# Optimization experiments

Measured on AMD Instinct MI355X. Metric: run time of the kernel, lower is better.

The kernel has to match this reference:

```python
import jax, jax.numpy as jnp
import numpy as np

B, C, H, T = 256, 2048, 1024, 64  # batch, code_num, hidden_dim, max_len


def setup_inputs() -> dict:
    key = jax.random.key(0)
    ks = jax.random.split(key, 7)
    s_ih = 1.0 / np.sqrt(C)
    s_hh = 1.0 / np.sqrt(H)
    return {
        "noise": jax.random.normal(ks[0], (B, H), dtype=jnp.float32),
        "W_ih": jax.random.uniform(ks[1], (3 * H, C), jnp.float32, -s_ih, s_ih),
        "b_ih": jax.random.uniform(ks[2], (3 * H,), jnp.float32, -s_ih, s_ih),
        "W_hh": jax.random.uniform(ks[3], (3 * H, H), jnp.float32, -s_hh, s_hh),
        "b_hh": jax.random.uniform(ks[4], (3 * H,), jnp.float32, -s_hh, s_hh),
        "W_out": jax.random.uniform(ks[5], (C, H), jnp.float32, -s_hh, s_hh),
        "b_out": jax.random.uniform(ks[6], (C,), jnp.float32, -s_hh, s_hh),
        "max_len": T,
    }


def reference(noise, W_ih, b_ih, W_hh, b_hh, W_out, b_out, max_len):
    # initial codes = sigmoid(Linear(noise))
    codes0 = jax.nn.sigmoid(noise @ W_out.T + b_out)  # [B, C]
    h0 = jnp.zeros((noise.shape[0], W_hh.shape[1]), dtype=noise.dtype)  # [B, H]

    def step(carry, _):
        codes, h = carry
        gi = codes @ W_ih.T + b_ih           # [B, 3H]
        gh = h @ W_hh.T + b_hh               # [B, 3H]
        i_r, i_z, i_n = jnp.split(gi, 3, axis=-1)
        h_r, h_z, h_n = jnp.split(gh, 3, axis=-1)
        r = jax.nn.sigmoid(i_r + h_r)
        z = jax.nn.sigmoid(i_z + h_z)
        n = jnp.tanh(i_n + r * h_n)
        h_new = (1.0 - z) * n + z * h        # PyTorch GRUCell update
        logits = h_new @ W_out.T + b_out
        codes_new = jax.nn.sigmoid(logits)
        # sample at step t is codes BEFORE the cell; hidden is h AFTER
        return (codes_new, h_new), (codes, h_new)

    _, (samples, hiddens) = jax.lax.scan(step, (codes0, h0), None, length=max_len)
    samples = jnp.swapaxes(samples, 0, 1)  # [B, T, C]
    hiddens = jnp.swapaxes(hiddens, 0, 1)  # [B, T, H]
    return samples, hiddens
```

## Files before the change

### kernel.cpp

```cpp
#include <hip/hip_runtime.h>
#include <hip/hip_bf16.h>

#define BB 256
#define CC 2048
#define HD 1024
#define TT 64
#define H3 3072

typedef __attribute__((ext_vector_type(8))) short bf16x8;
typedef __attribute__((ext_vector_type(4))) float f32x4;

__device__ __forceinline__ float sigmoidf_(float x){ return 1.0f/(1.0f+__expf(-x)); }
__device__ __forceinline__ float tanhf_(float x){ float e=__expf(2.0f*x); return 1.0f - 2.0f/(e+1.0f); }

__device__ __forceinline__ bf16x8 ldfrag(const __hip_bfloat16* p){
  return *reinterpret_cast<const bf16x8*>(p);
}
__device__ __forceinline__ unsigned short bfbits(float x){
  __hip_bfloat16 b = __float2bfloat16(x);
  return *reinterpret_cast<unsigned short*>(&b);
}

__global__ void cvt_f32_bf16(const float* __restrict__ in, __hip_bfloat16* __restrict__ out, int n){
  int i = (blockIdx.x*blockDim.x + threadIdx.x)*4;
  int stride = gridDim.x*blockDim.x*4;
  for (; i < n; i += stride){
    float4 v = *reinterpret_cast<const float4*>(in + i);
    ushort4 s;
    s.x = bfbits(v.x); s.y = bfbits(v.y); s.z = bfbits(v.z); s.w = bfbits(v.w);
    *reinterpret_cast<ushort4*>(out + i) = s;
  }
}

__global__ __launch_bounds__(1024, 4) void cell_kernel(
    const __hip_bfloat16* __restrict__ codes,
    const __hip_bfloat16* __restrict__ hprev,
    const __hip_bfloat16* __restrict__ Wih,
    const __hip_bfloat16* __restrict__ Whh,
    const float* __restrict__ bih,
    const float* __restrict__ bhh,
    float* __restrict__ hiddens,
    __hip_bfloat16* __restrict__ hnext,
    int t, int first)
{
  __shared__ float red[8*64*25];

  const int tid  = threadIdx.x;
  const int lane = tid & 63;
  const int wid  = tid >> 6;
  const int ws   = wid & 3;
  const int kc   = wid >> 2;
  const int bm   = blockIdx.x & 3;
  const int bj   = blockIdx.x >> 2;
  const int m0   = bm*64 + ws*16;
  const int j0   = bj*16;
  const int rl   = lane & 15;
  const int kg   = lane >> 4;

  const __hip_bfloat16* arow = codes + (size_t)(m0+rl)*CC + kc*512 + kg*8;
  const __hip_bfloat16* wr   = Wih   + (size_t)(j0+rl)*CC + kc*512 + kg*8;
  const __hip_bfloat16* wz   = wr + (size_t)HD*CC;
  const __hip_bfloat16* wn   = wz + (size_t)HD*CC;

  f32x4 zz4 = {0.f,0.f,0.f,0.f};
  f32x4 a0=zz4, a1=zz4, a2=zz4, a3=zz4, a4=zz4, a5=zz4;

#pragma unroll 4
  for (int k = 0; k < 512; k += 32){
    bf16x8 a  = ldfrag(arow + k);
    bf16x8 fr = ldfrag(wr + k);
    bf16x8 fz = ldfrag(wz + k);
    bf16x8 fn = ldfrag(wn + k);
    a0 = __builtin_amdgcn_mfma_f32_16x16x32_bf16(a, fr, a0, 0, 0, 0);
    a1 = __builtin_amdgcn_mfma_f32_16x16x32_bf16(a, fz, a1, 0, 0, 0);
    a2 = __builtin_amdgcn_mfma_f32_16x16x32_bf16(a, fn, a2, 0, 0, 0);
  }

  if (!first){
    const __hip_bfloat16* hrow = hprev + (size_t)(m0+rl)*HD + kc*256 + kg*8;
    const __hip_bfloat16* vr   = Whh   + (size_t)(j0+rl)*HD + kc*256 + kg*8;
    const __hip_bfloat16* vz   = vr + (size_t)HD*HD;
    const __hip_bfloat16* vn   = vz + (size_t)HD*HD;
#pragma unroll 4
    for (int k = 0; k < 256; k += 32){
      bf16x8 a  = ldfrag(hrow + k);
      bf16x8 fr = ldfrag(vr + k);
      bf16x8 fz = ldfrag(vz + k);
      bf16x8 fn = ldfrag(vn + k);
      a3 = __builtin_amdgcn_mfma_f32_16x16x32_bf16(a, fr, a3, 0, 0, 0);
      a4 = __builtin_amdgcn_mfma_f32_16x16x32_bf16(a, fz, a4, 0, 0, 0);
      a5 = __builtin_amdgcn_mfma_f32_16x16x32_bf16(a, fn, a5, 0, 0, 0);
    }
  }

  if (kc >= 2){
    float* p = &red[((kc-2)*4 + ws)*64*25 + lane*25];
#pragma unroll
    for (int q = 0; q < 4; q++){
      p[q] = a0[q]; p[4+q] = a1[q]; p[8+q] = a2[q];
      p[12+q] = a3[q]; p[16+q] = a4[q]; p[20+q] = a5[q];
    }
  }
  __syncthreads();
  if (kc < 2){
    const float* p = &red[(kc*4 + ws)*64*25 + lane*25];
#pragma unroll
    for (int q = 0; q < 4; q++){
      a0[q] += p[q]; a1[q] += p[4+q]; a2[q] += p[8+q];
      a3[q] += p[12+q]; a4[q] += p[16+q]; a5[q] += p[20+q];
    }
  }
  __syncthreads();
  if (kc == 1){
    float* p = &red[ws*64*25 + lane*25];
#pragma unroll
    for (int q = 0; q < 4; q++){
      p[q] = a0[q]; p[4+q] = a1[q]; p[8+q] = a2[q];
      p[12+q] = a3[q]; p[16+q] = a4[q]; p[20+q] = a5[q];
    }
  }
  __syncthreads();
  if (kc == 0){
    const float* p = &red[ws*64*25 + lane*25];
#pragma unroll
    for (int q = 0; q < 4; q++){
      a0[q] += p[q]; a1[q] += p[4+q]; a2[q] += p[8+q];
      a3[q] += p[12+q]; a4[q] += p[16+q]; a5[q] += p[20+q];
    }

    const int j = j0 + rl;
    const float bir = bih[j], biz = bih[j+HD], bin = bih[j+2*HD];
    const float bhr = bhh[j], bhz = bhh[j+HD], bhn = bhh[j+2*HD];
    const int rbase = m0 + kg*4;
#pragma unroll
    for (int q = 0; q < 4; q++){
      const int brow = rbase + q;
      float ir = a0[q] + bir, iz = a1[q] + biz, inn = a2[q] + bin;
      float hr = a3[q] + bhr, hz = a4[q] + bhz, hn = a5[q] + bhn;
      float r = sigmoidf_(ir + hr);
      float z = sigmoidf_(iz + hz);
      float n = tanhf_(inn + r*hn);
      float hp = first ? 0.0f : __bfloat162float(hprev[(size_t)brow*HD + j]);
      float hv = (1.0f - z)*n + z*hp;
      hiddens[(size_t)brow*TT*HD + (size_t)t*HD + j] = hv;
      hnext[(size_t)brow*HD + j] = __float2bfloat16(hv);
    }
  }
}

__global__ __launch_bounds__(1024, 4) void logits_kernel(
    const __hip_bfloat16* __restrict__ act,
    const __hip_bfloat16* __restrict__ Wout,
    const float* __restrict__ bout,
    float* __restrict__ samples,
    __hip_bfloat16* __restrict__ codes_out,
    int t)
{
  __shared__ float red[12*64*9];

  const int tid  = threadIdx.x;
  const int lane = tid & 63;
  const int wid  = tid >> 6;
  const int ws   = wid & 3;
  const int kc   = wid >> 2;
  const int bm   = blockIdx.x & 3;
  const int bc   = blockIdx.x >> 2;
  const int m0   = bm*64 + ws*16;
  const int c0   = bc*32;
  const int rl   = lane & 15;
  const int kg   = lane >> 4;

  const __hip_bfloat16* arow = act  + (size_t)(m0+rl)*HD + kc*256 + kg*8;
  const __hip_bfloat16* w0   = Wout + (size_t)(c0+rl)*HD + kc*256 + kg*8;
  const __hip_bfloat16* w1   = w0 + (size_t)16*HD;

  f32x4 zz4 = {0.f,0.f,0.f,0.f};
  f32x4 acc0 = zz4, acc1 = zz4;

#pragma unroll 4
  for (int k = 0; k < 256; k += 32){
    bf16x8 a  = ldfrag(arow + k);
    bf16x8 f0 = ldfrag(w0 + k);
    bf16x8 f1 = ldfrag(w1 + k);
    acc0 = __builtin_amdgcn_mfma_f32_16x16x32_bf16(a, f0, acc0, 0, 0, 0);
    acc1 = __builtin_amdgcn_mfma_f32_16x16x32_bf16(a, f1, acc1, 0, 0, 0);
  }

  if (kc >= 1){
    float* p = &red[((kc-1)*4 + ws)*64*9 + lane*9];
#pragma unroll
    for (int q = 0; q < 4; q++){ p[q] = acc0[q]; p[4+q] = acc1[q]; }
  }
  __syncthreads();
  if (kc == 0){
#pragma unroll
    for (int s = 0; s < 3; s++){
      const float* p = &red[(s*4 + ws)*64*9 + lane*9];
#pragma unroll
      for (int q = 0; q < 4; q++){ acc0[q] += p[q]; acc1[q] += p[4+q]; }
    }

    const int ca = c0 + rl, cb = ca + 16;
    const float b0 = bout[ca], b1 = bout[cb];
    const int rbase = m0 + kg*4;
#pragma unroll
    for (int q = 0; q < 4; q++){
      const int brow = rbase + q;
      float s0 = sigmoidf_(acc0[q] + b0);
      float s1 = sigmoidf_(acc1[q] + b1);
      samples[(size_t)brow*TT*CC + (size_t)t*CC + ca] = s0;
      samples[(size_t)brow*TT*CC + (size_t)t*CC + cb] = s1;
      codes_out[(size_t)brow*CC + ca] = __float2bfloat16(s0);
      codes_out[(size_t)brow*CC + cb] = __float2bfloat16(s1);
    }
  }
}

extern "C" void kernel_launch(void* const* d_in, const int* in_sizes, int n_in,
                              void* d_out, int out_size, void* d_ws, size_t ws_size,
                              hipStream_t stream) {
  const float* noise = (const float*)d_in[0];
  const float* W_ih  = (const float*)d_in[1];
  const float* b_ih  = (const float*)d_in[2];
  const float* W_hh  = (const float*)d_in[3];
  const float* b_hh  = (const float*)d_in[4];
  const float* W_out = (const float*)d_in[5];
  const float* b_out = (const float*)d_in[6];

  float* samples = (float*)d_out;
  float* hiddens = samples + (size_t)BB*TT*CC;

  char* w = (char*)d_ws;
  __hip_bfloat16* wih16 = (__hip_bfloat16*)w;  w += (size_t)H3*CC*2;
  __hip_bfloat16* whh16 = (__hip_bfloat16*)w;  w += (size_t)H3*HD*2;
  __hip_bfloat16* wout16= (__hip_bfloat16*)w;  w += (size_t)CC*HD*2;
  __hip_bfloat16* noise16=(__hip_bfloat16*)w;  w += (size_t)BB*HD*2;
  __hip_bfloat16* codes16=(__hip_bfloat16*)w;  w += (size_t)BB*CC*2;
  __hip_bfloat16* h16a  = (__hip_bfloat16*)w;  w += (size_t)BB*HD*2;
  __hip_bfloat16* h16b  = (__hip_bfloat16*)w;  w += (size_t)BB*HD*2;

  cvt_f32_bf16<<<2048, 256, 0, stream>>>(W_ih,  wih16,  H3*CC);
  cvt_f32_bf16<<<2048, 256, 0, stream>>>(W_hh,  whh16,  H3*HD);
  cvt_f32_bf16<<<1024, 256, 0, stream>>>(W_out, wout16, CC*HD);
  cvt_f32_bf16<<<256,  256, 0, stream>>>(noise, noise16, BB*HD);

  logits_kernel<<<256, 1024, 0, stream>>>(noise16, wout16, b_out, samples, codes16, 0);

  for (int t = 0; t < TT; t++){
    __hip_bfloat16* hprev = (t & 1) ? h16a : h16b;
    __hip_bfloat16* hnext = (t & 1) ? h16b : h16a;
    cell_kernel<<<256, 1024, 0, stream>>>(codes16, hprev, wih16, whh16,
                                          b_ih, b_hh, hiddens, hnext,
                                          t, (t == 0) ? 1 : 0);
    if (t < TT-1){
      logits_kernel<<<256, 1024, 0, stream>>>(hnext, wout16, b_out,
                                              samples, codes16, t+1);
    }
  }
}
```

Baseline: 3.796 ms.

## Fuse per-step GRU and logits kernels into one persistent kernel with grid barriers

Replaces about 128 separate launches of the cell and logits kernels with a single persistent kernel of 256 blocks. The kernel loops over time steps and separates phases with a software grid barrier built on atomics. Block indexing changes so each block owns a fixed batch tile and column slice, which keeps its bias loads in registers across steps. This is meant to remove kernel launch overhead and inter-kernel gaps. It relies on all 256 blocks being co-resident (one per CU on MI355X), otherwise the barrier deadlocks, and the barrier itself adds spin latency.

```diff
diff --git a/kernel.cpp b/kernel.cpp
--- a/kernel.cpp
+++ b/kernel.cpp
@@ -6,13 +6,13 @@
 #define HD 1024
 #define TT 64
 #define H3 3072
+#define NBLK 256
 
 typedef __attribute__((ext_vector_type(8))) short bf16x8;
 typedef __attribute__((ext_vector_type(4))) float f32x4;
 
 __device__ __forceinline__ float sigmoidf_(float x){ return 1.0f/(1.0f+__expf(-x)); }
 __device__ __forceinline__ float tanhf_(float x){ float e=__expf(2.0f*x); return 1.0f - 2.0f/(e+1.0f); }
-
 __device__ __forceinline__ bf16x8 ldfrag(const __hip_bfloat16* p){
   return *reinterpret_cast<const bf16x8*>(p);
 }
@@ -32,16 +32,40 @@
   }
 }
 
-__global__ __launch_bounds__(1024, 4) void cell_kernel(
-    const __hip_bfloat16* __restrict__ codes,
-    const __hip_bfloat16* __restrict__ hprev,
-    const __hip_bfloat16* __restrict__ Wih,
-    const __hip_bfloat16* __restrict__ Whh,
+__device__ __forceinline__ void gridbar(unsigned* cnt, unsigned* gen){
+  __syncthreads();
+  if (threadIdx.x == 0){
+    __threadfence();
+    unsigned g = __hip_atomic_load(gen, __ATOMIC_RELAXED, __HIP_MEMORY_SCOPE_AGENT);
+    unsigned a = __hip_atomic_fetch_add(cnt, 1u, __ATOMIC_ACQ_REL, __HIP_MEMORY_SCOPE_AGENT);
+    if (a == NBLK-1u){
+      __hip_atomic_store(cnt, 0u, __ATOMIC_RELAXED, __HIP_MEMORY_SCOPE_AGENT);
+      __hip_atomic_store(gen, g+1u, __ATOMIC_RELEASE, __HIP_MEMORY_SCOPE_AGENT);
+    } else {
+      while (__hip_atomic_load(gen, __ATOMIC_RELAXED, __HIP_MEMORY_SCOPE_AGENT) == g){
+        __builtin_amdgcn_s_sleep(2);
+      }
+    }
+    __threadfence();
+  }
+  __syncthreads();
+}
+
+#define MFMA(a,b,c) __builtin_amdgcn_mfma_f32_16x16x32_bf16((a),(b),(c),0,0,0)
+
+__global__ __launch_bounds__(1024, 4) void gru_persistent(
+    const __hip_bfloat16* __restrict__ wih,
+    const __hip_bfloat16* __restrict__ whh,
+    const __hip_bfloat16* __restrict__ wout,
+    const __hip_bfloat16* __restrict__ noise16,
     const float* __restrict__ bih,
     const float* __restrict__ bhh,
+    const float* __restrict__ bout,
+    float* __restrict__ samples,
     float* __restrict__ hiddens,
-    __hip_bfloat16* __restrict__ hnext,
-    int t, int first)
+    __hip_bfloat16* codes16,
+    __hip_bfloat16* h16a, __hip_bfloat16* h16b,
+    unsigned* bar)
 {
   __shared__ float red[8*64*25];
 
@@ -50,168 +74,157 @@
   const int wid  = tid >> 6;
   const int ws   = wid & 3;
   const int kc   = wid >> 2;
-  const int bm   = blockIdx.x & 3;
-  const int bj   = blockIdx.x >> 2;
+  const int bm   = blockIdx.x >> 6;
+  const int bsub = blockIdx.x & 63;
   const int m0   = bm*64 + ws*16;
-  const int j0   = bj*16;
   const int rl   = lane & 15;
   const int kg   = lane >> 4;
-
-  const __hip_bfloat16* arow = codes + (size_t)(m0+rl)*CC + kc*512 + kg*8;
-  const __hip_bfloat16* wr   = Wih   + (size_t)(j0+rl)*CC + kc*512 + kg*8;
-  const __hip_bfloat16* wz   = wr + (size_t)HD*CC;
-  const __hip_bfloat16* wn   = wz + (size_t)HD*CC;
-
-  f32x4 zz4 = {0.f,0.f,0.f,0.f};
-  f32x4 a0=zz4, a1=zz4, a2=zz4, a3=zz4, a4=zz4, a5=zz4;
-
-#pragma unroll 4
-  for (int k = 0; k < 512; k += 32){
-    bf16x8 a  = ldfrag(arow + k);
-    bf16x8 fr = ldfrag(wr + k);
-    bf16x8 fz = ldfrag(wz + k);
-    bf16x8 fn = ldfrag(wn + k);
-    a0 = __builtin_amdgcn_mfma_f32_16x16x32_bf16(a, fr, a0, 0, 0, 0);
-    a1 = __builtin_amdgcn_mfma_f32_16x16x32_bf16(a, fz, a1, 0, 0, 0);
-    a2 = __builtin_amdgcn_mfma_f32_16x16x32_bf16(a, fn, a2, 0, 0, 0);
-  }
-
-  if (!first){
-    const __hip_bfloat16* hrow = hprev + (size_t)(m0+rl)*HD + kc*256 + kg*8;
-    const __hip_bfloat16* vr   = Whh   + (size_t)(j0+rl)*HD + kc*256 + kg*8;
-    const __hip_bfloat16* vz   = vr + (size_t)HD*HD;
-    const __hip_bfloat16* vn   = vz + (size_t)HD*HD;
+  unsigned* cnt = bar;
+  unsigned* gen = bar + 32;
+
+  const int jA  = bsub*16 + rl;
+  const int caB = bsub*32 + rl;
+  const int cbB = caB + 16;
+  const float bir = bih[jA], biz = bih[jA+HD], bin = bih[jA+2*HD];
+  const float bhr = bhh[jA], bhz = bhh[jA+HD], bhn = bhh[jA+2*HD];
+  const float b0 = bout[caB], b1 = bout[cbB];
+  const int rbase = m0 + kg*4;
+
+  auto phaseB = [&](const __hip_bfloat16* act, int t){
+    const __hip_bfloat16* arow = act  + (size_t)(m0+rl)*HD + kc*256 + kg*8;
+    const __hip_bfloat16* w0   = wout + (size_t)(bsub*32+rl)*HD + kc*256 + kg*8;
+    const __hip_bfloat16* w1   = w0 + (size_t)16*HD;
+    f32x4 acc0 = {0.f,0.f,0.f,0.f}, acc1 = {0.f,0.f,0.f,0.f};
 #pragma unroll 4
     for (int k = 0; k < 256; k += 32){
-      bf16x8 a  = ldfrag(hrow + k);
-      bf16x8 fr = ldfrag(vr + k);
-      bf16x8 fz = ldfrag(vz + k);
-      bf16x8 fn = ldfrag(vn + k);
-      a3 = __builtin_amdgcn_mfma_f32_16x16x32_bf16(a, fr, a3, 0, 0, 0);
-      a4 = __builtin_amdgcn_mfma_f32_16x16x32_bf16(a, fz, a4, 0, 0, 0);
-      a5 = __builtin_amdgcn_mfma_f32_16x16x32_bf16(a, fn, a5, 0, 0, 0);
-    }
-  }
-
-  if (kc >= 2){
-    float* p = &red[((kc-2)*4 + ws)*64*25 + lane*25];
-#pragma unroll
-    for (int q = 0; q < 4; q++){
-      p[q] = a0[q]; p[4+q] = a1[q]; p[8+q] = a2[q];
-      p[12+q] = a3[q]; p[16+q] = a4[q]; p[20+q] = a5[q];
-    }
-  }
-  __syncthreads();
-  if (kc < 2){
-    const float* p = &red[(kc*4 + ws)*64*25 + lane*25];
-#pragma unroll
-    for (int q = 0; q < 4; q++){
-      a0[q] += p[q]; a1[q] += p[4+q]; a2[q] += p[8+q];
-      a3[q] += p[12+q]; a4[q] += p[16+q]; a5[q] += p[20+q];
-    }
-  }
-  __syncthreads();
-  if (kc == 1){
-    float* p = &red[ws*64*25 + lane*25];
-#pragma unroll
-    for (int q = 0; q < 4; q++){
-      p[q] = a0[q]; p[4+q] = a1[q]; p[8+q] = a2[q];
-      p[12+q] = a3[q]; p[16+q] = a4[q]; p[20+q] = a5[q];
-    }
-  }
-  __syncthreads();
-  if (kc == 0){
-    const float* p = &red[ws*64*25 + lane*25];
-#pragma unroll
-    for (int q = 0; q < 4; q++){
-      a0[q] += p[q]; a1[q] += p[4+q]; a2[q] += p[8+q];
-      a3[q] += p[12+q]; a4[q] += p[16+q]; a5[q] += p[20+q];
-    }
-
-    const int j = j0 + rl;
-    const float bir = bih[j], biz = bih[j+HD], bin = bih[j+2*HD];
-    const float bhr = bhh[j], bhz = bhh[j+HD], bhn = bhh[j+2*HD];
-    const int rbase = m0 + kg*4;
-#pragma unroll
-    for (int q = 0; q < 4; q++){
-      const int brow = rbase + q;
-      float ir = a0[q] + bir, iz = a1[q] + biz, inn = a2[q] + bin;
-      float hr = a3[q] + bhr, hz = a4[q] + bhz, hn = a5[q] + bhn;
-      float r = sigmoidf_(ir + hr);
-      float z = sigmoidf_(iz + hz);
-      float n = tanhf_(inn + r*hn);
-      float hp = first ? 0.0f : __bfloat162float(hprev[(size_t)brow*HD + j]);
-      float hv = (1.0f - z)*n + z*hp;
-      hiddens[(size_t)brow*TT*HD + (size_t)t*HD + j] = hv;
-      hnext[(size_t)brow*HD + j] = __float2bfloat16(hv);
-    }
-  }
-}
-
-__global__ __launch_bounds__(1024, 4) void logits_kernel(
-    const __hip_bfloat16* __restrict__ act,
-    const __hip_bfloat16* __restrict__ Wout,
-    const float* __restrict__ bout,
-    float* __restrict__ samples,
-    __hip_bfloat16* __restrict__ codes_out,
-    int t)
-{
-  __shared__ float red[12*64*9];
-
-  const int tid  = threadIdx.x;
-  const int lane = tid & 63;
-  const int wid  = tid >> 6;
-  const int ws   = wid & 3;
-  const int kc   = wid >> 2;
-  const int bm   = blockIdx.x & 3;
-  const int bc   = blockIdx.x >> 2;
-  const int m0   = bm*64 + ws*16;
-  const int c0   = bc*32;
-  const int rl   = lane & 15;
-  const int kg   = lane >> 4;
-
-  const __hip_bfloat16* arow = act  + (size_t)(m0+rl)*HD + kc*256 + kg*8;
-  const __hip_bfloat16* w0   = Wout + (size_t)(c0+rl)*HD + kc*256 + kg*8;
-  const __hip_bfloat16* w1   = w0 + (size_t)16*HD;
-
-  f32x4 zz4 = {0.f,0.f,0.f,0.f};
-  f32x4 acc0 = zz4, acc1 = zz4;
-
+      bf16x8 a  = ldfrag(arow + k);
+      bf16x8 f0 = ldfrag(w0 + k);
+      bf16x8 f1 = ldfrag(w1 + k);
+      acc0 = MFMA(a, f0, acc0);
+      acc1 = MFMA(a, f1, acc1);
+    }
+    if (kc >= 1){
+      float* p = &red[((kc-1)*4 + ws)*64*9 + lane*9];
+#pragma unroll
+      for (int q = 0; q < 4; q++){ p[q] = acc0[q]; p[4+q] = acc1[q]; }
+    }
+    __syncthreads();
+    if (kc == 0){
+#pragma unroll
+      for (int s = 0; s < 3; s++){
+        const float* p = &red[(s*4 + ws)*64*9 + lane*9];
+#pragma unroll
+        for (int q = 0; q < 4; q++){ acc0[q] += p[q]; acc1[q] += p[4+q]; }
+      }
+#pragma unroll
+      for (int q = 0; q < 4; q++){
+        const int brow = rbase + q;
+        float s0 = sigmoidf_(acc0[q] + b0);
+        float s1 = sigmoidf_(acc1[q] + b1);
+        samples[(size_t)brow*TT*CC + (size_t)t*CC + caB] = s0;
+        samples[(size_t)brow*TT*CC + (size_t)t*CC + cbB] = s1;
+        codes16[(size_t)brow*CC + caB] = __float2bfloat16(s0);
+        codes16[(size_t)brow*CC + cbB] = __float2bfloat16(s1);
+      }
+    }
+  };
+
+  auto phaseA = [&](const __hip_bfloat16* hprev, __hip_bfloat16* hnext,
+                    int t, int first){
+    const __hip_bfloat16* arow = codes16 + (size_t)(m0+rl)*CC + kc*512 + kg*8;
+    const __hip_bfloat16* wr   = wih     + (size_t)(bsub*16+rl)*CC + kc*512 + kg*8;
+    const __hip_bfloat16* wz   = wr + (size_t)HD*CC;
+    const __hip_bfloat16* wn   = wz + (size_t)HD*CC;
+    f32x4 zz4 = {0.f,0.f,0.f,0.f};
+    f32x4 a0=zz4, a1=zz4, a2=zz4, a3=zz4, a4=zz4, a5=zz4;
 #pragma unroll 4
-  for (int k = 0; k < 256; k += 32){
-    bf16x8 a  = ldfrag(arow + k);
-    bf16x8 f0 = ldfrag(w0 + k);
-    bf16x8 f1 = ldfrag(w1 + k);
-    acc0 = __builtin_amdgcn_mfma_f32_16x16x32_bf16(a, f0, acc0, 0, 0, 0);
-    acc1 = __builtin_amdgcn_mfma_f32_16x16x32_bf16(a, f1, acc1, 0, 0, 0);
-  }
-
-  if (kc >= 1){
-    float* p = &red[((kc-1)*4 + ws)*64*9 + lane*9];
-#pragma unroll
-    for (int q = 0; q < 4; q++){ p[q] = acc0[q]; p[4+q] = acc1[q]; }
-  }
-  __syncthreads();
-  if (kc == 0){
-#pragma unroll
-    for (int s = 0; s < 3; s++){
-      const float* p = &red[(s*4 + ws)*64*9 + lane*9];
-#pragma unroll
-      for (int q = 0; q < 4; q++){ acc0[q] += p[q]; acc1[q] += p[4+q]; }
-    }
-
-    const int ca = c0 + rl, cb = ca + 16;
-    const float b0 = bout[ca], b1 = bout[cb];
-    const int rbase = m0 + kg*4;
-#pragma unroll
-    for (int q = 0; q < 4; q++){
-      const int brow = rbase + q;
-      float s0 = sigmoidf_(acc0[q] + b0);
-      float s1 = sigmoidf_(acc1[q] + b1);
-      samples[(size_t)brow*TT*CC + (size_t)t*CC + ca] = s0;
-      samples[(size_t)brow*TT*CC + (size_t)t*CC + cb] = s1;
-      codes_out[(size_t)brow*CC + ca] = __float2bfloat16(s0);
-      codes_out[(size_t)brow*CC + cb] = __float2bfloat16(s1);
+    for (int k = 0; k < 512; k += 32){
+      bf16x8 a  = ldfrag(arow + k);
+      bf16x8 fr = ldfrag(wr + k);
+      bf16x8 fz = ldfrag(wz + k);
+      bf16x8 fn = ldfrag(wn + k);
+      a0 = MFMA(a, fr, a0);
+      a1 = MFMA(a, fz, a1);
+      a2 = MFMA(a, fn, a2);
+    }
+    if (!first){
+      const __hip_bfloat16* hrow = hprev + (size_t)(m0+rl)*HD + kc*256 + kg*8;
+      const __hip_bfloat16* vr   = whh   + (size_t)(bsub*16+rl)*HD + kc*256 + kg*8;
+      const __hip_bfloat16* vz   = vr + (size_t)HD*HD;
+      const __hip_bfloat16* vn   = vz + (size_t)HD*HD;
+#pragma unroll 4
+      for (int k = 0; k < 256; k += 32){
+        bf16x8 a  = ldfrag(hrow + k);
+        bf16x8 fr = ldfrag(vr + k);
+        bf16x8 fz = ldfrag(vz + k);
+        bf16x8 fn = ldfrag(vn + k);
+        a3 = MFMA(a, fr, a3);
+        a4 = MFMA(a, fz, a4);
+        a5 = MFMA(a, fn, a5);
+      }
+    }
+    if (kc >= 2){
+      float* p = &red[((kc-2)*4 + ws)*64*25 + lane*25];
+#pragma unroll
+      for (int q = 0; q < 4; q++){
+        p[q] = a0[q]; p[4+q] = a1[q]; p[8+q] = a2[q];
+        p[12+q] = a3[q]; p[16+q] = a4[q]; p[20+q] = a5[q];
+      }
+    }
+    __syncthreads();
+    if (kc < 2){
+      const float* p = &red[(kc*4 + ws)*64*25 + lane*25];
+#pragma unroll
+      for (int q = 0; q < 4; q++){
+        a0[q] += p[q]; a1[q] += p[4+q]; a2[q] += p[8+q];
+        a3[q] += p[12+q]; a4[q] += p[16+q]; a5[q] += p[20+q];
+      }
+    }
+    __syncthreads();
+    if (kc == 1){
+      float* p = &red[ws*64*25 + lane*25];
+#pragma unroll
+      for (int q = 0; q < 4; q++){
+        p[q] = a0[q]; p[4+q] = a1[q]; p[8+q] = a2[q];
+        p[12+q] = a3[q]; p[16+q] = a4[q]; p[20+q] = a5[q];
+      }
+    }
+    __syncthreads();
+    if (kc == 0){
+      const float* p = &red[ws*64*25 + lane*25];
+#pragma unroll
+      for (int q = 0; q < 4; q++){
+        a0[q] += p[q]; a1[q] += p[4+q]; a2[q] += p[8+q];
+        a3[q] += p[12+q]; a4[q] += p[16+q]; a5[q] += p[20+q];
+      }
+#pragma unroll
+      for (int q = 0; q < 4; q++){
+        const int brow = rbase + q;
+        float ir = a0[q] + bir, iz = a1[q] + biz, inn = a2[q] + bin;
+        float hr = a3[q] + bhr, hz = a4[q] + bhz, hn = a5[q] + bhn;
+        float r = sigmoidf_(ir + hr);
+        float z = sigmoidf_(iz + hz);
+        float n = tanhf_(inn + r*hn);
+        float hp = first ? 0.0f : __bfloat162float(hprev[(size_t)brow*HD + jA]);
+        float hv = (1.0f - z)*n + z*hp;
+        hiddens[(size_t)brow*TT*HD + (size_t)t*HD + jA] = hv;
+        hnext[(size_t)brow*HD + jA] = __float2bfloat16(hv);
+      }
+    }
+  };
+
+  phaseB(noise16, 0);
+  gridbar(cnt, gen);
+
+#pragma unroll 1
+  for (int t = 0; t < TT; t++){
+    __hip_bfloat16* hprev = (t & 1) ? h16a : h16b;
+    __hip_bfloat16* hnext = (t & 1) ? h16b : h16a;
+    phaseA(hprev, hnext, t, (t == 0) ? 1 : 0);
+    gridbar(cnt, gen);
+    if (t < TT-1){
+      phaseB(hnext, t+1);
+      gridbar(cnt, gen);
     }
   }
 }
@@ -231,6 +244,7 @@
   float* hiddens = samples + (size_t)BB*TT*CC;
 
   char* w = (char*)d_ws;
+  unsigned* bar = (unsigned*)w;                w += 256;
   __hip_bfloat16* wih16 = (__hip_bfloat16*)w;  w += (size_t)H3*CC*2;
   __hip_bfloat16* whh16 = (__hip_bfloat16*)w;  w += (size_t)H3*HD*2;
   __hip_bfloat16* wout16= (__hip_bfloat16*)w;  w += (size_t)CC*HD*2;
@@ -239,22 +253,13 @@
   __hip_bfloat16* h16a  = (__hip_bfloat16*)w;  w += (size_t)BB*HD*2;
   __hip_bfloat16* h16b  = (__hip_bfloat16*)w;  w += (size_t)BB*HD*2;
 
+  hipMemsetAsync(bar, 0, 256, stream);
   cvt_f32_bf16<<<2048, 256, 0, stream>>>(W_ih,  wih16,  H3*CC);
   cvt_f32_bf16<<<2048, 256, 0, stream>>>(W_hh,  whh16,  H3*HD);
   cvt_f32_bf16<<<1024, 256, 0, stream>>>(W_out, wout16, CC*HD);
   cvt_f32_bf16<<<256,  256, 0, stream>>>(noise, noise16, BB*HD);
 
-  logits_kernel<<<256, 1024, 0, stream>>>(noise16, wout16, b_out, samples, codes16, 0);
-
-  for (int t = 0; t < TT; t++){
-    __hip_bfloat16* hprev = (t & 1) ? h16a : h16b;
-    __hip_bfloat16* hnext = (t & 1) ? h16b : h16a;
-    cell_kernel<<<256, 1024, 0, stream>>>(codes16, hprev, wih16, whh16,
-                                          b_ih, b_hh, hiddens, hnext,
-                                          t, (t == 0) ? 1 : 0);
-    if (t < TT-1){
-      logits_kernel<<<256, 1024, 0, stream>>>(hnext, wout16, b_out,
-                                              samples, codes16, t+1);
-    }
-  }
-}
+  gru_persistent<<<NBLK, 1024, 0, stream>>>(
+      wih16, whh16, wout16, noise16, b_ih, b_hh, b_out,
+      samples, hiddens, codes16, h16a, h16b, bar);
+}
```

New measurement: 6.146 ms. +61.9%, slower.
